# Performance work log

Hardware: AMD Instinct MI355X
Metric: run time of the kernel (lower is better)

Reference implementation:

```python
import jax, jax.numpy as jnp
import numpy as np

E = 1024   # embed_dim
H = 16     # num_heads
D = E // H # head dim = 64
NUM_BUCKETS = 32
MAX_DISTANCE = 128


def _relative_position_bucket(rel, num_buckets=NUM_BUCKETS, max_distance=MAX_DISTANCE):
    # T5-style bucketing (bidirectional): sign half + log-spaced far buckets.
    nb = num_buckets // 2
    buckets = (rel > 0).astype(jnp.int32) * nb
    rel = jnp.abs(rel)
    max_exact = nb // 2
    is_small = rel < max_exact
    # clamp to >=1 before log to avoid -inf on the masked-out branch
    rel_f = jnp.maximum(rel, 1).astype(jnp.float32)
    large = max_exact + (
        jnp.log(rel_f / max_exact) / np.log(max_distance / max_exact) * (nb - max_exact)
    ).astype(jnp.int32)
    large = jnp.minimum(large, nb - 1)
    return buckets + jnp.where(is_small, rel, large)


def setup_inputs() -> dict:
    key = jax.random.key(0)
    ks = jax.random.split(key, 6)
    B, S, K = 2, 2048, 2048
    w = 0.02
    return {
        "hidden_states": jax.random.normal(ks[0], (B, S, E), jnp.float32),
        "key_value_states": jax.random.normal(ks[1], (B, K, E), jnp.float32),
        "Wq": jax.random.normal(ks[2], (E, E), jnp.float32) * w,
        "Wkv": jax.random.normal(ks[3], (E, 2 * E), jnp.float32) * w,
        "Wo": jax.random.normal(ks[4], (E, E), jnp.float32) * w,
        "rel_bias": jax.random.normal(ks[5], (NUM_BUCKETS, H), jnp.float32) * w,
    }


def reference(hidden_states, key_value_states, Wq, Wkv, Wo, rel_bias):
    B, S, _ = hidden_states.shape
    K = key_value_states.shape[1]
    # projections (no bias, no 1/sqrt(d) scaling — T5 style)
    q = (hidden_states @ Wq).reshape(B, S, H, D).transpose(0, 2, 1, 3)      # [B,H,S,D]
    kv = (key_value_states @ Wkv).reshape(B, K, 2, H, D)
    k = kv[:, :, 0].transpose(0, 2, 1, 3)                                   # [B,H,K,D]
    v = kv[:, :, 1].transpose(0, 2, 1, 3)                                   # [B,H,K,D]
    scores = jnp.einsum('bhsd,bhkd->bhsk', q, k)                            # [B,H,S,K]
    # relative position bias
    rel = jnp.arange(K)[None, :] - jnp.arange(S)[:, None]                   # [S,K]
    buckets = _relative_position_bucket(rel)                                # [S,K]
    bias = rel_bias[buckets].transpose(2, 0, 1)[None]                       # [1,H,S,K]
    scores = scores + bias
    attn = jax.nn.softmax(scores.astype(jnp.float32), axis=-1).astype(scores.dtype)
    out = jnp.einsum('bhsk,bhkd->bshd', attn, v).reshape(B, S, E)
    return out @ Wo
```

## Files before the change

kernel.cpp:

```cpp
#include <hip/hip_runtime.h>
#include <hip/hip_bf16.h>
#include <math.h>

typedef __hip_bfloat16 bf16;
typedef __bf16 bf16x4 __attribute__((ext_vector_type(4)));
typedef __bf16 bf16x8 __attribute__((ext_vector_type(8)));
typedef float f32x4 __attribute__((ext_vector_type(4)));
typedef float f32x16 __attribute__((ext_vector_type(16)));
typedef unsigned short us4 __attribute__((ext_vector_type(4)));

__device__ inline __bf16 f2b(float f) {
  __hip_bfloat16 h = __float2bfloat16(f);
  return *reinterpret_cast<__bf16*>(&h);
}
__device__ inline unsigned short b2u(float f) {
  __hip_bfloat16 h = __float2bfloat16(f);
  return *reinterpret_cast<unsigned short*>(&h);
}
__device__ inline bf16x8 ld16(const bf16* p) {
  bf16x4 lo = *(const bf16x4*)p;
  bf16x4 hi = *(const bf16x4*)(p + 4);
  return __builtin_shufflevector(lo, hi, 0, 1, 2, 3, 4, 5, 6, 7);
}
__device__ inline void st16(bf16* p, uint4 v) {
  *(uint2*)p = make_uint2(v.x, v.y);
  *(uint2*)(p + 4) = make_uint2(v.z, v.w);
}
__device__ inline void async16(const bf16* g, bf16* l) {
  __builtin_amdgcn_global_load_lds(
      (const __attribute__((address_space(1))) unsigned int*)g,
      (__attribute__((address_space(3))) unsigned int*)l, 16, 0, 0);
}

__global__ void transpose_cast_k(const float* __restrict__ in, bf16* __restrict__ out,
                                 int rows, int cols) {
  __shared__ float tile[32][33];
  int c0 = blockIdx.x * 32;
  int r0 = blockIdx.y * 32;
  int tx = threadIdx.x;
  int ty = threadIdx.y;
  for (int i = ty; i < 32; i += 8)
    tile[i][tx] = in[(size_t)(r0 + i) * cols + c0 + tx];
  __syncthreads();
  for (int i = ty; i < 32; i += 8)
    out[(size_t)(c0 + i) * rows + r0 + tx] = __float2bfloat16(tile[tx][i]);
}

__global__ void bias_lut_k(const float* __restrict__ rel_bias, float* __restrict__ lut) {
  int r = blockIdx.x * blockDim.x + threadIdx.x;
  if (r >= 4096) return;
  int rel = r - 2048;
  int b = rel > 0 ? 16 : 0;
  int ar = rel < 0 ? -rel : rel;
  int idx;
  if (ar < 8) {
    idx = b + ar;
  } else {
    double t = log((double)ar / 8.0) / log(16.0) * 8.0;
    int lg = 8 + (int)t;
    if (lg > 15) lg = 15;
    idx = b + lg;
  }
  for (int h = 0; h < 16; ++h)
    lut[h * 4096 + r] = rel_bias[idx * 16 + h];
}

#define LDA 44
__global__ __launch_bounds__(256) void gemm_qkv_k(const float* __restrict__ hidden,
                                                  const float* __restrict__ kvs,
                                                  const bf16* __restrict__ WqT,
                                                  const bf16* __restrict__ WkvT,
                                                  bf16* __restrict__ Qb,
                                                  bf16* __restrict__ Kb,
                                                  bf16* __restrict__ Vt) {
  __shared__ __align__(16) bf16 As[128 * LDA];
  __shared__ __align__(16) bf16 Bs[128 * 32];
  const int tid = threadIdx.x;
  const int lane = tid & 63;
  const int w = tid >> 6;
  const int wm = (w >> 1) * 64;
  const int wn = (w & 1) * 64;
  const int l15 = lane & 15;
  const int quad = lane >> 4;
  const int srow = lane >> 2;
  const int skg = lane & 3;

  const bool isQ = blockIdx.y < 8;
  const float* A = isQ ? hidden : kvs;
  const bf16* Bt = isQ ? WqT : WkvT;
  const int n0 = (isQ ? blockIdx.y : blockIdx.y - 8) * 128;
  const int m0 = blockIdx.x * 128;

  f32x4 acc[4][4];
#pragma unroll
  for (int i = 0; i < 4; ++i)
#pragma unroll
    for (int j = 0; j < 4; ++j) acc[i][j] = (f32x4){0.f, 0.f, 0.f, 0.f};

  for (int k0 = 0; k0 < 1024; k0 += 32) {
    __syncthreads();
#pragma unroll
    for (int rep = 0; rep < 2; ++rep) {
      int seg = w * 2 + rep;
      async16(Bt + (size_t)(n0 + seg * 16 + srow) * 1024 + k0 + skg * 8, Bs + seg * 512);
    }
#pragma unroll
    for (int rep = 0; rep < 2; ++rep) {
      int slot = tid + rep * 256;
      int row = slot >> 2, kg = slot & 3;
      const float* pa = A + (size_t)(m0 + row) * 1024 + k0 + kg * 8;
      float4 a0 = *(const float4*)pa;
      float4 a1 = *(const float4*)(pa + 4);
      bf16x4 lo, hi;
      lo[0] = f2b(a0.x); lo[1] = f2b(a0.y); lo[2] = f2b(a0.z); lo[3] = f2b(a0.w);
      hi[0] = f2b(a1.x); hi[1] = f2b(a1.y); hi[2] = f2b(a1.z); hi[3] = f2b(a1.w);
      bf16* dst = As + row * LDA + kg * 8;
      *(bf16x4*)dst = lo;
      *(bf16x4*)(dst + 4) = hi;
    }
    __syncthreads();
    bf16x8 af[4], bfr[4];
#pragma unroll
    for (int i = 0; i < 4; ++i)
      af[i] = ld16(As + (wm + i * 16 + l15) * LDA + quad * 8);
#pragma unroll
    for (int j = 0; j < 4; ++j)
      bfr[j] = *(const bf16x8*)(Bs + (wn + j * 16 + l15) * 32 + quad * 8);
#pragma unroll
    for (int i = 0; i < 4; ++i)
#pragma unroll
      for (int j = 0; j < 4; ++j)
        acc[i][j] = __builtin_amdgcn_mfma_f32_16x16x32_bf16(af[i], bfr[j], acc[i][j], 0, 0, 0);
  }

  if (!isQ && n0 >= 1024) {
#pragma unroll
    for (int i = 0; i < 4; ++i) {
      int gmb = m0 + wm + i * 16 + quad * 4;
      int b = gmb >> 11, kp = gmb & 2047;
#pragma unroll
      for (int j = 0; j < 4; ++j) {
        int gn = n0 + wn + j * 16 + l15;
        int h = (gn >> 6) & 15, d = gn & 63;
        us4 pk;
#pragma unroll
        for (int r = 0; r < 4; ++r) pk[r] = b2u(acc[i][j][r]);
        *(us4*)(Vt + ((((size_t)b * 16 + h) * 64 + d) << 11) + kp) = pk;
      }
    }
    return;
  }
#pragma unroll
  for (int i = 0; i < 4; ++i) {
#pragma unroll
    for (int j = 0; j < 4; ++j) {
#pragma unroll
      for (int r = 0; r < 4; ++r) {
        int gm = m0 + wm + i * 16 + quad * 4 + r;
        int gn = n0 + wn + j * 16 + l15;
        bf16 v = __float2bfloat16(acc[i][j][r]);
        int b = gm >> 11, s = gm & 2047;
        int h = (gn >> 6) & 15, d = gn & 63;
        bf16* dst = isQ ? Qb : Kb;
        dst[((((size_t)b * 16 + h) * 2048 + s) << 6) + d] = v;
      }
    }
  }
}

__global__ __launch_bounds__(256) void gemm_o_k(const bf16* __restrict__ A,
                                                const bf16* __restrict__ Bt,
                                                float* __restrict__ C0) {
  __shared__ __align__(16) bf16 As[128 * 32];
  __shared__ __align__(16) bf16 Bs[128 * 32];
  const int tid = threadIdx.x;
  const int lane = tid & 63;
  const int w = tid >> 6;
  const int wm = (w >> 1) * 64;
  const int wn = (w & 1) * 64;
  const int m0 = blockIdx.x * 128;
  const int n0 = blockIdx.y * 128;
  const int l15 = lane & 15;
  const int quad = lane >> 4;
  const int srow = lane >> 2;
  const int skg = lane & 3;

  f32x4 acc[4][4];
#pragma unroll
  for (int i = 0; i < 4; ++i)
#pragma unroll
    for (int j = 0; j < 4; ++j) acc[i][j] = (f32x4){0.f, 0.f, 0.f, 0.f};

  for (int k0 = 0; k0 < 1024; k0 += 32) {
    __syncthreads();
#pragma unroll
    for (int rep = 0; rep < 2; ++rep) {
      int seg = w * 2 + rep;
      async16(A + (size_t)(m0 + seg * 16 + srow) * 1024 + k0 + skg * 8, As + seg * 512);
      async16(Bt + (size_t)(n0 + seg * 16 + srow) * 1024 + k0 + skg * 8, Bs + seg * 512);
    }
    __syncthreads();
    bf16x8 af[4], bfr[4];
#pragma unroll
    for (int i = 0; i < 4; ++i)
      af[i] = *(const bf16x8*)(As + (wm + i * 16 + l15) * 32 + quad * 8);
#pragma unroll
    for (int j = 0; j < 4; ++j)
      bfr[j] = *(const bf16x8*)(Bs + (wn + j * 16 + l15) * 32 + quad * 8);
#pragma unroll
    for (int i = 0; i < 4; ++i)
#pragma unroll
      for (int j = 0; j < 4; ++j)
        acc[i][j] = __builtin_amdgcn_mfma_f32_16x16x32_bf16(af[i], bfr[j], acc[i][j], 0, 0, 0);
  }
#pragma unroll
  for (int i = 0; i < 4; ++i)
#pragma unroll
    for (int j = 0; j < 4; ++j)
#pragma unroll
      for (int r = 0; r < 4; ++r) {
        int gm = m0 + wm + i * 16 + quad * 4 + r;
        int gn = n0 + wn + j * 16 + l15;
        C0[(size_t)gm * 1024 + gn] = acc[i][j][r];
      }
}

#define STK 68
__global__ __launch_bounds__(256) void attn_k(const bf16* __restrict__ Qb,
                                              const bf16* __restrict__ Kb,
                                              const bf16* __restrict__ Vt,
                                              const float* __restrict__ lut,
                                              bf16* __restrict__ Ob) {
  __shared__ __align__(16) bf16 Ks[64 * STK];
  __shared__ __align__(16) bf16 Vs[64 * STK];
  __shared__ __align__(16) bf16 Ps[128 * STK];
  __shared__ float lbias[2180];

  const int tid = threadIdx.x;
  const int lane = tid & 63;
  const int w = tid >> 6;
  const int q31 = lane & 31;
  const int half = lane >> 5;

  const int qt = blockIdx.x;
  const int bh = blockIdx.y;
  const int h = bh & 15, b = bh >> 4;
  const int qb = qt * 128;

  const int gcap = h * 4096 + 4095;
  const int gbase = h * 4096 + 1921 - qb;
  for (int t = tid; t < 2176; t += 256) {
    int gi = gbase + t;
    lbias[t] = lut[gi > gcap ? gcap : gi];
  }

  const size_t base = (size_t)bh * 2048 * 64;
  const size_t vbase = (size_t)bh * 64 * 2048;
  const int qg = qb + w * 32 + q31;

  bf16x8 qf[4];
#pragma unroll
  for (int c = 0; c < 4; ++c)
    qf[c] = *(const bf16x8*)(Qb + base + (size_t)qg * 64 + c * 16 + half * 8);

  f32x16 oacc[2];
#pragma unroll
  for (int dj = 0; dj < 2; ++dj)
#pragma unroll
    for (int r = 0; r < 16; ++r) oacc[dj][r] = 0.f;
  float m_run = -INFINITY, l_run = 0.f;

  bf16* prow = Ps + (w * 32 + q31) * STK;

  for (int kt = 0; kt < 2048; kt += 64) {
    __syncthreads();
#pragma unroll
    for (int rep = 0; rep < 2; ++rep) {
      int slot = tid + rep * 256;
      int rr = slot >> 3, cg = slot & 7;
      uint4 kv = *(const uint4*)(Kb + base + (size_t)(kt + rr) * 64 + cg * 8);
      st16(Ks + rr * STK + cg * 8, kv);
      uint4 vv = *(const uint4*)(Vt + vbase + (size_t)rr * 2048 + kt + cg * 8);
      st16(Vs + rr * STK + cg * 8, vv);
    }
    __syncthreads();

    f32x16 sacc[2];
#pragma unroll
    for (int mt = 0; mt < 2; ++mt) {
#pragma unroll
      for (int r = 0; r < 16; ++r) sacc[mt][r] = 0.f;
#pragma unroll
      for (int c = 0; c < 4; ++c) {
        bf16x8 kf = ld16(Ks + (mt * 32 + q31) * STK + c * 16 + half * 8);
        sacc[mt] = __builtin_amdgcn_mfma_f32_32x32x16_bf16(kf, qf[c], sacc[mt], 0, 0, 0);
      }
    }

    const int xoff = kt + 127 - w * 32 - q31 + 4 * half;
    float mx = -INFINITY;
#pragma unroll
    for (int mt = 0; mt < 2; ++mt)
#pragma unroll
      for (int g = 0; g < 4; ++g) {
        int x0 = xoff + mt * 32 + 8 * g;
#pragma unroll
        for (int rr = 0; rr < 4; ++rr) {
          float s = sacc[mt][4 * g + rr] + lbias[x0 + rr];
          sacc[mt][4 * g + rr] = s;
          mx = fmaxf(mx, s);
        }
      }
    mx = fmaxf(mx, __shfl_xor(mx, 32));
    float mnew = fmaxf(m_run, mx);
    float alpha = __expf(m_run - mnew);
    m_run = mnew;
    float sum = 0.f;
#pragma unroll
    for (int mt = 0; mt < 2; ++mt)
#pragma unroll
      for (int r = 0; r < 16; ++r) {
        float p = __expf(sacc[mt][r] - mnew);
        sacc[mt][r] = p;
        sum += p;
      }
    sum += __shfl_xor(sum, 32);
    l_run = l_run * alpha + sum;

#pragma unroll
    for (int mt = 0; mt < 2; ++mt)
#pragma unroll
      for (int g = 0; g < 4; ++g) {
        us4 pk;
#pragma unroll
        for (int rr = 0; rr < 4; ++rr) pk[rr] = b2u(sacc[mt][4 * g + rr]);
        *(us4*)(prow + mt * 32 + 8 * g + 4 * half) = pk;
      }

#pragma unroll
    for (int dj = 0; dj < 2; ++dj)
#pragma unroll
      for (int r = 0; r < 16; ++r) oacc[dj][r] *= alpha;

    bf16x8 pf[4];
#pragma unroll
    for (int c = 0; c < 4; ++c) pf[c] = ld16(prow + c * 16 + half * 8);
#pragma unroll
    for (int dj = 0; dj < 2; ++dj)
#pragma unroll
      for (int c = 0; c < 4; ++c) {
        bf16x8 vf = ld16(Vs + (dj * 32 + q31) * STK + c * 16 + half * 8);
        oacc[dj] = __builtin_amdgcn_mfma_f32_32x32x16_bf16(vf, pf[c], oacc[dj], 0, 0, 0);
      }
  }

  float inv = 1.0f / l_run;
  float* dummy;
  (void)dummy;
#pragma unroll
  for (int dj = 0; dj < 2; ++dj)
#pragma unroll
    for (int g = 0; g < 4; ++g) {
      us4 pk;
#pragma unroll
      for (int rr = 0; rr < 4; ++rr) pk[rr] = b2u(oacc[dj][4 * g + rr] * inv);
      int d0 = dj * 32 + 8 * g + 4 * half;
      *(us4*)(Ob + ((size_t)(b * 2048 + qg)) * 1024 + h * 64 + d0) = pk;
    }
}

extern "C" void kernel_launch(void* const* d_in, const int* in_sizes, int n_in,
                              void* d_out, int out_size, void* d_ws, size_t ws_size,
                              hipStream_t stream) {
  const float* hidden = (const float*)d_in[0];
  const float* kvs    = (const float*)d_in[1];
  const float* Wq     = (const float*)d_in[2];
  const float* Wkv    = (const float*)d_in[3];
  const float* Wo     = (const float*)d_in[4];
  const float* relb   = (const float*)d_in[5];
  float* out = (float*)d_out;

  char* ws = (char*)d_ws;
  bf16* WqT  = (bf16*)(ws + (size_t)0);
  bf16* WkvT = (bf16*)(ws + ((size_t)2 << 20));
  bf16* WoT  = (bf16*)(ws + ((size_t)6 << 20));
  bf16* Ob   = (bf16*)(ws + ((size_t)8 << 20));
  bf16* Qb   = (bf16*)(ws + ((size_t)16 << 20));
  bf16* Kb   = (bf16*)(ws + ((size_t)24 << 20));
  bf16* Vt   = (bf16*)(ws + ((size_t)32 << 20));
  float* LUT = (float*)(ws + ((size_t)40 << 20));

  dim3 tb(32, 8);
  transpose_cast_k<<<dim3(32, 32), tb, 0, stream>>>(Wq, WqT, 1024, 1024);
  transpose_cast_k<<<dim3(64, 32), tb, 0, stream>>>(Wkv, WkvT, 1024, 2048);
  transpose_cast_k<<<dim3(32, 32), tb, 0, stream>>>(Wo, WoT, 1024, 1024);
  bias_lut_k<<<16, 256, 0, stream>>>(relb, LUT);

  gemm_qkv_k<<<dim3(32, 24), 256, 0, stream>>>(hidden, kvs, WqT, WkvT, Qb, Kb, Vt);
  attn_k<<<dim3(16, 32), 256, 0, stream>>>(Qb, Kb, Vt, LUT, Ob);
  gemm_o_k<<<dim3(32, 8), 256, 0, stream>>>(Ob, WoT, out);
}
```

Measured before the change: 272.0 us.

## Pre-cast activations to bf16, use exp2 softmax, widen attention key tile, retile O-proj

Hidden and key/value activations are cast to bf16 in separate kernels, so the QKV GEMM can stream A through async global-to-LDS loads instead of converting fp32 inline. Softmax moves to exp2, with log2e folded into Q and the bias LUT, and uses a cheaper rounding bf16 pack. The attention key tile doubles to 128 to halve the number of barriers and rescales. The output GEMM uses 128x64 tiles for more blocks. This adds two extra launches plus an extra pass over the activations, and reuses the output and O buffers as scratch.

```diff
diff --git a/kernel.cpp b/kernel.cpp
--- a/kernel.cpp
+++ b/kernel.cpp
@@ -9,6 +9,18 @@
 typedef float f32x16 __attribute__((ext_vector_type(16)));
 typedef unsigned short us4 __attribute__((ext_vector_type(4)));
 
+#define LOG2E 1.44269504088896340736f
+
+#if defined(__has_builtin)
+#if __has_builtin(__builtin_amdgcn_exp2f)
+#define EXP2(x) __builtin_amdgcn_exp2f(x)
+#else
+#define EXP2(x) exp2f(x)
+#endif
+#else
+#define EXP2(x) exp2f(x)
+#endif
+
 __device__ inline __bf16 f2b(float f) {
   __hip_bfloat16 h = __float2bfloat16(f);
   return *reinterpret_cast<__bf16*>(&h);
@@ -16,6 +28,11 @@
 __device__ inline unsigned short b2u(float f) {
   __hip_bfloat16 h = __float2bfloat16(f);
   return *reinterpret_cast<unsigned short*>(&h);
+}
+__device__ inline unsigned short b2u_fast(float f) {
+  union { float f; unsigned u; } v;
+  v.f = f;
+  return (unsigned short)((v.u + 0x8000u) >> 16);
 }
 __device__ inline bf16x8 ld16(const bf16* p) {
   bf16x4 lo = *(const bf16x4*)p;
@@ -30,6 +47,17 @@
   __builtin_amdgcn_global_load_lds(
       (const __attribute__((address_space(1))) unsigned int*)g,
       (__attribute__((address_space(3))) unsigned int*)l, 16, 0, 0);
+}
+
+__global__ void cast_k(const float* __restrict__ in, bf16* __restrict__ out, int n) {
+  int i = (blockIdx.x * 256 + threadIdx.x) * 8;
+  if (i >= n) return;
+  float4 a0 = *(const float4*)(in + i);
+  float4 a1 = *(const float4*)(in + i + 4);
+  bf16x8 v;
+  v[0] = f2b(a0.x); v[1] = f2b(a0.y); v[2] = f2b(a0.z); v[3] = f2b(a0.w);
+  v[4] = f2b(a1.x); v[5] = f2b(a1.y); v[6] = f2b(a1.z); v[7] = f2b(a1.w);
+  *(bf16x8*)(out + i) = v;
 }
 
 __global__ void transpose_cast_k(const float* __restrict__ in, bf16* __restrict__ out,
@@ -62,18 +90,17 @@
     idx = b + lg;
   }
   for (int h = 0; h < 16; ++h)
-    lut[h * 4096 + r] = rel_bias[idx * 16 + h];
-}
-
-#define LDA 44
-__global__ __launch_bounds__(256) void gemm_qkv_k(const float* __restrict__ hidden,
-                                                  const float* __restrict__ kvs,
+    lut[h * 4096 + r] = rel_bias[idx * 16 + h] * LOG2E;
+}
+
+__global__ __launch_bounds__(256) void gemm_qkv_k(const bf16* __restrict__ hbf,
+                                                  const bf16* __restrict__ kbf,
                                                   const bf16* __restrict__ WqT,
                                                   const bf16* __restrict__ WkvT,
                                                   bf16* __restrict__ Qb,
                                                   bf16* __restrict__ Kb,
                                                   bf16* __restrict__ Vt) {
-  __shared__ __align__(16) bf16 As[128 * LDA];
+  __shared__ __align__(16) bf16 As[128 * 32];
   __shared__ __align__(16) bf16 Bs[128 * 32];
   const int tid = threadIdx.x;
   const int lane = tid & 63;
@@ -86,7 +113,7 @@
   const int skg = lane & 3;
 
   const bool isQ = blockIdx.y < 8;
-  const float* A = isQ ? hidden : kvs;
+  const bf16* A = isQ ? hbf : kbf;
   const bf16* Bt = isQ ? WqT : WkvT;
   const int n0 = (isQ ? blockIdx.y : blockIdx.y - 8) * 128;
   const int m0 = blockIdx.x * 128;
@@ -102,27 +129,14 @@
 #pragma unroll
     for (int rep = 0; rep < 2; ++rep) {
       int seg = w * 2 + rep;
+      async16(A + (size_t)(m0 + seg * 16 + srow) * 1024 + k0 + skg * 8, As + seg * 512);
       async16(Bt + (size_t)(n0 + seg * 16 + srow) * 1024 + k0 + skg * 8, Bs + seg * 512);
     }
-#pragma unroll
-    for (int rep = 0; rep < 2; ++rep) {
-      int slot = tid + rep * 256;
-      int row = slot >> 2, kg = slot & 3;
-      const float* pa = A + (size_t)(m0 + row) * 1024 + k0 + kg * 8;
-      float4 a0 = *(const float4*)pa;
-      float4 a1 = *(const float4*)(pa + 4);
-      bf16x4 lo, hi;
-      lo[0] = f2b(a0.x); lo[1] = f2b(a0.y); lo[2] = f2b(a0.z); lo[3] = f2b(a0.w);
-      hi[0] = f2b(a1.x); hi[1] = f2b(a1.y); hi[2] = f2b(a1.z); hi[3] = f2b(a1.w);
-      bf16* dst = As + row * LDA + kg * 8;
-      *(bf16x4*)dst = lo;
-      *(bf16x4*)(dst + 4) = hi;
-    }
     __syncthreads();
     bf16x8 af[4], bfr[4];
 #pragma unroll
     for (int i = 0; i < 4; ++i)
-      af[i] = ld16(As + (wm + i * 16 + l15) * LDA + quad * 8);
+      af[i] = *(const bf16x8*)(As + (wm + i * 16 + l15) * 32 + quad * 8);
 #pragma unroll
     for (int j = 0; j < 4; ++j)
       bfr[j] = *(const bf16x8*)(Bs + (wn + j * 16 + l15) * 32 + quad * 8);
@@ -150,44 +164,42 @@
     }
     return;
   }
-#pragma unroll
-  for (int i = 0; i < 4; ++i) {
-#pragma unroll
-    for (int j = 0; j < 4; ++j) {
+  const float scale = isQ ? LOG2E : 1.0f;
+#pragma unroll
+  for (int i = 0; i < 4; ++i)
+#pragma unroll
+    for (int j = 0; j < 4; ++j)
 #pragma unroll
       for (int r = 0; r < 4; ++r) {
         int gm = m0 + wm + i * 16 + quad * 4 + r;
         int gn = n0 + wn + j * 16 + l15;
-        bf16 v = __float2bfloat16(acc[i][j][r]);
+        bf16 v = __float2bfloat16(acc[i][j][r] * scale);
         int b = gm >> 11, s = gm & 2047;
         int h = (gn >> 6) & 15, d = gn & 63;
         bf16* dst = isQ ? Qb : Kb;
         dst[((((size_t)b * 16 + h) * 2048 + s) << 6) + d] = v;
       }
-    }
-  }
 }
 
 __global__ __launch_bounds__(256) void gemm_o_k(const bf16* __restrict__ A,
                                                 const bf16* __restrict__ Bt,
                                                 float* __restrict__ C0) {
   __shared__ __align__(16) bf16 As[128 * 32];
-  __shared__ __align__(16) bf16 Bs[128 * 32];
+  __shared__ __align__(16) bf16 Bs[64 * 32];
   const int tid = threadIdx.x;
   const int lane = tid & 63;
   const int w = tid >> 6;
-  const int wm = (w >> 1) * 64;
-  const int wn = (w & 1) * 64;
+  const int wm = w * 32;
   const int m0 = blockIdx.x * 128;
-  const int n0 = blockIdx.y * 128;
+  const int n0 = blockIdx.y * 64;
   const int l15 = lane & 15;
   const int quad = lane >> 4;
   const int srow = lane >> 2;
   const int skg = lane & 3;
 
-  f32x4 acc[4][4];
-#pragma unroll
-  for (int i = 0; i < 4; ++i)
+  f32x4 acc[2][4];
+#pragma unroll
+  for (int i = 0; i < 2; ++i)
 #pragma unroll
     for (int j = 0; j < 4; ++j) acc[i][j] = (f32x4){0.f, 0.f, 0.f, 0.f};
 
@@ -197,44 +209,45 @@
     for (int rep = 0; rep < 2; ++rep) {
       int seg = w * 2 + rep;
       async16(A + (size_t)(m0 + seg * 16 + srow) * 1024 + k0 + skg * 8, As + seg * 512);
-      async16(Bt + (size_t)(n0 + seg * 16 + srow) * 1024 + k0 + skg * 8, Bs + seg * 512);
-    }
-    __syncthreads();
-    bf16x8 af[4], bfr[4];
-#pragma unroll
-    for (int i = 0; i < 4; ++i)
+    }
+    async16(Bt + (size_t)(n0 + w * 16 + srow) * 1024 + k0 + skg * 8, Bs + w * 512);
+    __syncthreads();
+    bf16x8 af[2], bfr[4];
+#pragma unroll
+    for (int i = 0; i < 2; ++i)
       af[i] = *(const bf16x8*)(As + (wm + i * 16 + l15) * 32 + quad * 8);
 #pragma unroll
     for (int j = 0; j < 4; ++j)
-      bfr[j] = *(const bf16x8*)(Bs + (wn + j * 16 + l15) * 32 + quad * 8);
-#pragma unroll
-    for (int i = 0; i < 4; ++i)
+      bfr[j] = *(const bf16x8*)(Bs + (j * 16 + l15) * 32 + quad * 8);
+#pragma unroll
+    for (int i = 0; i < 2; ++i)
 #pragma unroll
       for (int j = 0; j < 4; ++j)
         acc[i][j] = __builtin_amdgcn_mfma_f32_16x16x32_bf16(af[i], bfr[j], acc[i][j], 0, 0, 0);
   }
 #pragma unroll
-  for (int i = 0; i < 4; ++i)
+  for (int i = 0; i < 2; ++i)
 #pragma unroll
     for (int j = 0; j < 4; ++j)
 #pragma unroll
       for (int r = 0; r < 4; ++r) {
         int gm = m0 + wm + i * 16 + quad * 4 + r;
-        int gn = n0 + wn + j * 16 + l15;
+        int gn = n0 + j * 16 + l15;
         C0[(size_t)gm * 1024 + gn] = acc[i][j][r];
       }
 }
 
 #define STK 68
+#define SVK 136
 __global__ __launch_bounds__(256) void attn_k(const bf16* __restrict__ Qb,
                                               const bf16* __restrict__ Kb,
                                               const bf16* __restrict__ Vt,
                                               const float* __restrict__ lut,
                                               bf16* __restrict__ Ob) {
-  __shared__ __align__(16) bf16 Ks[64 * STK];
-  __shared__ __align__(16) bf16 Vs[64 * STK];
-  __shared__ __align__(16) bf16 Ps[128 * STK];
-  __shared__ float lbias[2180];
+  __shared__ float lbias[2176];
+  __shared__ __align__(16) bf16 Ks[128 * STK];
+  __shared__ __align__(16) bf16 Vs[64 * SVK];
+  __shared__ __align__(16) bf16 Ps[128 * SVK];
 
   const int tid = threadIdx.x;
   const int lane = tid & 63;
@@ -247,12 +260,8 @@
   const int h = bh & 15, b = bh >> 4;
   const int qb = qt * 128;
 
-  const int gcap = h * 4096 + 4095;
   const int gbase = h * 4096 + 1921 - qb;
-  for (int t = tid; t < 2176; t += 256) {
-    int gi = gbase + t;
-    lbias[t] = lut[gi > gcap ? gcap : gi];
-  }
+  for (int t = tid; t < 2175; t += 256) lbias[t] = lut[gbase + t];
 
   const size_t base = (size_t)bh * 2048 * 64;
   const size_t vbase = (size_t)bh * 64 * 2048;
@@ -270,24 +279,25 @@
     for (int r = 0; r < 16; ++r) oacc[dj][r] = 0.f;
   float m_run = -INFINITY, l_run = 0.f;
 
-  bf16* prow = Ps + (w * 32 + q31) * STK;
-
-  for (int kt = 0; kt < 2048; kt += 64) {
-    __syncthreads();
-#pragma unroll
-    for (int rep = 0; rep < 2; ++rep) {
+  bf16* prow = Ps + (w * 32 + q31) * SVK;
+
+  for (int kt = 0; kt < 2048; kt += 128) {
+    __syncthreads();
+#pragma unroll
+    for (int rep = 0; rep < 4; ++rep) {
       int slot = tid + rep * 256;
-      int rr = slot >> 3, cg = slot & 7;
-      uint4 kv = *(const uint4*)(Kb + base + (size_t)(kt + rr) * 64 + cg * 8);
-      st16(Ks + rr * STK + cg * 8, kv);
-      uint4 vv = *(const uint4*)(Vt + vbase + (size_t)rr * 2048 + kt + cg * 8);
-      st16(Vs + rr * STK + cg * 8, vv);
-    }
-    __syncthreads();
-
-    f32x16 sacc[2];
-#pragma unroll
-    for (int mt = 0; mt < 2; ++mt) {
+      int kk = slot >> 3, cg = slot & 7;
+      uint4 kv = *(const uint4*)(Kb + base + (size_t)(kt + kk) * 64 + cg * 8);
+      st16(Ks + kk * STK + cg * 8, kv);
+      int d = slot >> 4, c = slot & 15;
+      uint4 vv = *(const uint4*)(Vt + vbase + (size_t)d * 2048 + kt + c * 8);
+      st16(Vs + d * SVK + c * 8, vv);
+    }
+    __syncthreads();
+
+    f32x16 sacc[4];
+#pragma unroll
+    for (int mt = 0; mt < 4; ++mt) {
 #pragma unroll
       for (int r = 0; r < 16; ++r) sacc[mt][r] = 0.f;
 #pragma unroll
@@ -297,13 +307,13 @@
       }
     }
 
-    const int xoff = kt + 127 - w * 32 - q31 + 4 * half;
+    const int xbase = kt + 127 + 4 * half - w * 32 - q31;
     float mx = -INFINITY;
 #pragma unroll
-    for (int mt = 0; mt < 2; ++mt)
+    for (int mt = 0; mt < 4; ++mt)
 #pragma unroll
       for (int g = 0; g < 4; ++g) {
-        int x0 = xoff + mt * 32 + 8 * g;
+        int x0 = xbase + mt * 32 + 8 * g;
 #pragma unroll
         for (int rr = 0; rr < 4; ++rr) {
           float s = sacc[mt][4 * g + rr] + lbias[x0 + rr];
@@ -313,14 +323,14 @@
       }
     mx = fmaxf(mx, __shfl_xor(mx, 32));
     float mnew = fmaxf(m_run, mx);
-    float alpha = __expf(m_run - mnew);
+    float alpha = EXP2(m_run - mnew);
     m_run = mnew;
     float sum = 0.f;
 #pragma unroll
-    for (int mt = 0; mt < 2; ++mt)
+    for (int mt = 0; mt < 4; ++mt)
 #pragma unroll
       for (int r = 0; r < 16; ++r) {
-        float p = __expf(sacc[mt][r] - mnew);
+        float p = EXP2(sacc[mt][r] - mnew);
         sacc[mt][r] = p;
         sum += p;
       }
@@ -328,12 +338,12 @@
     l_run = l_run * alpha + sum;
 
 #pragma unroll
-    for (int mt = 0; mt < 2; ++mt)
+    for (int mt = 0; mt < 4; ++mt)
 #pragma unroll
       for (int g = 0; g < 4; ++g) {
         us4 pk;
 #pragma unroll
-        for (int rr = 0; rr < 4; ++rr) pk[rr] = b2u(sacc[mt][4 * g + rr]);
+        for (int rr = 0; rr < 4; ++rr) pk[rr] = b2u_fast(sacc[mt][4 * g + rr]);
         *(us4*)(prow + mt * 32 + 8 * g + 4 * half) = pk;
       }
 
@@ -342,21 +352,19 @@
 #pragma unroll
       for (int r = 0; r < 16; ++r) oacc[dj][r] *= alpha;
 
-    bf16x8 pf[4];
-#pragma unroll
-    for (int c = 0; c < 4; ++c) pf[c] = ld16(prow + c * 16 + half * 8);
+    bf16x8 pf[8];
+#pragma unroll
+    for (int c = 0; c < 8; ++c) pf[c] = ld16(prow + c * 16 + half * 8);
 #pragma unroll
     for (int dj = 0; dj < 2; ++dj)
 #pragma unroll
-      for (int c = 0; c < 4; ++c) {
-        bf16x8 vf = ld16(Vs + (dj * 32 + q31) * STK + c * 16 + half * 8);
+      for (int c = 0; c < 8; ++c) {
+        bf16x8 vf = ld16(Vs + (dj * 32 + q31) * SVK + c * 16 + half * 8);
         oacc[dj] = __builtin_amdgcn_mfma_f32_32x32x16_bf16(vf, pf[c], oacc[dj], 0, 0, 0);
       }
   }
 
   float inv = 1.0f / l_run;
-  float* dummy;
-  (void)dummy;
 #pragma unroll
   for (int dj = 0; dj < 2; ++dj)
 #pragma unroll
@@ -385,18 +393,22 @@
   bf16* WkvT = (bf16*)(ws + ((size_t)2 << 20));
   bf16* WoT  = (bf16*)(ws + ((size_t)6 << 20));
   bf16* Ob   = (bf16*)(ws + ((size_t)8 << 20));
+  bf16* hbf  = Ob;
   bf16* Qb   = (bf16*)(ws + ((size_t)16 << 20));
   bf16* Kb   = (bf16*)(ws + ((size_t)24 << 20));
   bf16* Vt   = (bf16*)(ws + ((size_t)32 << 20));
   float* LUT = (float*)(ws + ((size_t)40 << 20));
+  bf16* kbf  = (bf16*)d_out;
 
   dim3 tb(32, 8);
   transpose_cast_k<<<dim3(32, 32), tb, 0, stream>>>(Wq, WqT, 1024, 1024);
   transpose_cast_k<<<dim3(64, 32), tb, 0, stream>>>(Wkv, WkvT, 1024, 2048);
   transpose_cast_k<<<dim3(32, 32), tb, 0, stream>>>(Wo, WoT, 1024, 1024);
   bias_lut_k<<<16, 256, 0, stream>>>(relb, LUT);
-
-  gemm_qkv_k<<<dim3(32, 24), 256, 0, stream>>>(hidden, kvs, WqT, WkvT, Qb, Kb, Vt);
+  cast_k<<<2048, 256, 0, stream>>>(hidden, hbf, 4194304);
+  cast_k<<<2048, 256, 0, stream>>>(kvs, kbf, 4194304);
+
+  gemm_qkv_k<<<dim3(32, 24), 256, 0, stream>>>(hbf, kbf, WqT, WkvT, Qb, Kb, Vt);
   attn_k<<<dim3(16, 32), 256, 0, stream>>>(Qb, Kb, Vt, LUT, Ob);
-  gemm_o_k<<<dim3(32, 8), 256, 0, stream>>>(Ob, WoT, out);
-}
+  gemm_o_k<<<dim3(32, 16), 256, 0, stream>>>(Ob, WoT, out);
+}
```

After: 253.0 us. 1.08x faster.
